# Kernel optimization log

Hardware: AMD Instinct MI355X
Metric: run time of the kernel (lower is better)

## Reference

```python
import jax, jax.numpy as jnp
import numpy as np

N_NODES = 8192
N_EDGES = 65536


def _segment_softmax(scores, seg_ids, num_segments):
    # scores: [E, 1], seg_ids: [E] -> softmax over edges sharing the same dst
    m = jax.ops.segment_max(scores, seg_ids, num_segments=num_segments)  # [N,1]
    e = jnp.exp(scores - m[seg_ids])
    denom = jax.ops.segment_sum(e, seg_ids, num_segments=num_segments)   # [N,1]
    return e / denom[seg_ids]


def setup_inputs() -> dict:
    key = jax.random.key(0)
    ks = jax.random.split(key, 12)
    s = lambda fin: 1.0 / np.sqrt(fin)
    inp = {
        'n_f': jax.random.normal(ks[0], (N_NODES, 1024), jnp.float32),
        'word2vec': jax.random.normal(ks[1], (N_NODES, 300), jnp.float32),
        's_f': jax.random.normal(ks[2], (N_EDGES, 16), jnp.float32),
        'src': jax.random.randint(ks[3], (N_EDGES,), 0, N_NODES),
        'dst': jax.random.randint(ks[4], (N_EDGES,), 0, N_NODES),
        'We': jax.random.normal(ks[5], (2064, 1024), jnp.float32) * s(2064),
        'be': jnp.zeros((1024,), jnp.float32),
        'Wel': jax.random.normal(ks[6], (600, 600), jnp.float32) * s(600),
        'bel': jnp.zeros((600,), jnp.float32),
        'Wa': jax.random.normal(ks[7], (1024, 1), jnp.float32) * s(1024),
        'ba': jnp.zeros((1,), jnp.float32),
        'Wal': jax.random.normal(ks[8], (600, 1), jnp.float32) * s(600),
        'bal': jnp.zeros((1,), jnp.float32),
        'Wn': jax.random.normal(ks[9], (2048, 1024), jnp.float32) * s(2048),
        'bn': jnp.zeros((1024,), jnp.float32),
        'Wnl': jax.random.normal(ks[10], (600, 300), jnp.float32) * s(600),
        'bnl': jnp.zeros((300,), jnp.float32),
    }
    return inp


def reference(n_f, word2vec, s_f, src, dst,
              We, be, Wel, bel, Wa, ba, Wal, bal, Wn, bn, Wnl, bnl):
    # ---- edge apply (H_H_EdgeApplyModule) ----
    src_nf = n_f[src]                                    # [E,1024] gather
    feat = jnp.concatenate([src_nf, s_f, n_f[dst]], axis=1)  # [E,2064]
    e_f = jax.nn.relu(feat @ We + be)                    # [E,1024]
    feat_lang = jnp.concatenate([word2vec[src], word2vec[dst]], axis=1)  # [E,600]
    e_f_lang = jax.nn.relu(feat_lang @ Wel + bel)        # [E,600]

    # ---- edge attention (E_AttentionModule1): scalar score per edge ----
    a_feat = e_f @ Wa + ba                               # [E,1]
    a_feat_lang = e_f_lang @ Wal + bal                   # [E,1]

    # ---- reduce: mailbox softmax over incoming edges per dst node ----
    alpha = _segment_softmax(a_feat, dst, N_NODES)       # [E,1]
    alpha_lang = _segment_softmax(a_feat_lang, dst, N_NODES)
    z_f = jax.ops.segment_sum(alpha * (src_nf + e_f), dst, num_segments=N_NODES)      # [N,1024]
    z_f_lang = jax.ops.segment_sum(alpha_lang * word2vec[src], dst, num_segments=N_NODES)  # [N,300]

    # ---- node apply (H_NodeApplyModule) ----
    new_n_f = jax.nn.relu(jnp.concatenate([n_f, z_f], axis=1) @ Wn + bn)              # [N,1024]
    new_n_f_lang = jax.nn.relu(jnp.concatenate([word2vec, z_f_lang], axis=1) @ Wnl + bnl)  # [N,300]
    return new_n_f, new_n_f_lang
```

## Files before the change

### kernel.cpp

```cpp
#include <hip/hip_runtime.h>
#include <hip/hip_bf16.h>

#define N_NODES 8192
#define N_EDGES 65536
#define OUT0_ELEMS ((size_t)N_NODES * 1024)

using bf16 = __hip_bfloat16;
typedef __attribute__((ext_vector_type(8))) short short8;
typedef __attribute__((ext_vector_type(4))) float f32x4;

__device__ __forceinline__ float b2f(bf16 x) { return __bfloat162float(x); }
__device__ __forceinline__ bf16 f2b(float x) { return __float2bfloat16(x); }
__device__ __forceinline__ unsigned short bbits(float x)
{
  union { bf16 h; unsigned short u; } v; v.h = f2b(x); return v.u;
}
__device__ __forceinline__ unsigned pack2(float a, float b)
{
  return (unsigned)bbits(a) | ((unsigned)bbits(b) << 16);
}
__device__ __forceinline__ float4 cvt2x(uint2 u)
{
  float4 r;
  r.x = __uint_as_float(u.x << 16);
  r.y = __uint_as_float(u.x & 0xffff0000u);
  r.z = __uint_as_float(u.y << 16);
  r.w = __uint_as_float(u.y & 0xffff0000u);
  return r;
}
__device__ __forceinline__ float4 ld4b(const bf16* p)
{
  uint2 u = *(const uint2*)p;
  return cvt2x(u);
}
__device__ __forceinline__ void st4b(bf16* p, float a, float b, float c, float d)
{
  uint2 v; v.x = pack2(a, b); v.y = pack2(c, d);
  *(uint2*)p = v;
}

__global__ void GNN_27650999451833_kernel() {}

__global__ void gnn6_zero(int* __restrict__ p, int n)
{
  int i = blockIdx.x * blockDim.x + threadIdx.x;
  if (i < n) p[i] = 0;
}

__global__ __launch_bounds__(256)
void gnn7_cvt(const float* __restrict__ src, bf16* __restrict__ dst, int n8)
{
  int i = blockIdx.x * blockDim.x + threadIdx.x;
  if (i < n8) {
    float4 a = ((const float4*)src)[2 * i];
    float4 b = ((const float4*)src)[2 * i + 1];
    uint4 p;
    p.x = pack2(a.x, a.y); p.y = pack2(a.z, a.w);
    p.z = pack2(b.x, b.y); p.w = pack2(b.z, b.w);
    ((uint4*)dst)[i] = p;
  }
}

__global__ __launch_bounds__(256)
void gnn8_pad_w2v(const float* __restrict__ src, bf16* __restrict__ dst)
{
  int idx = blockIdx.x * blockDim.x + threadIdx.x;
  if (idx >= N_NODES * 80) return;
  int r = idx / 80, c0 = (idx % 80) * 4;
  float v[4];
#pragma unroll
  for (int j = 0; j < 4; ++j) {
    int c = c0 + j;
    v[j] = (c < 300) ? src[(size_t)r * 300 + c] : 0.f;
  }
  uint2 p; p.x = pack2(v[0], v[1]); p.y = pack2(v[2], v[3]);
  *(uint2*)(dst + (size_t)r * 320 + c0) = p;
}

__global__ __launch_bounds__(256)
void gnn12_sf_pad(const float* __restrict__ s_f, bf16* __restrict__ sf_pad)
{
  int e = blockIdx.x * 256 + threadIdx.x;
  if (e >= N_EDGES) return;
  const float4* sp = (const float4*)(s_f + (size_t)e * 16);
  float4 s0 = sp[0], s1 = sp[1], s2 = sp[2], s3 = sp[3];
  uint4 lo, hi;
  lo.x = pack2(s0.x, s0.y); lo.y = pack2(s0.z, s0.w);
  lo.z = pack2(s1.x, s1.y); lo.w = pack2(s1.z, s1.w);
  hi.x = pack2(s2.x, s2.y); hi.y = pack2(s2.z, s2.w);
  hi.z = pack2(s3.x, s3.y); hi.w = pack2(s3.z, s3.w);
  uint4* dp = (uint4*)(sf_pad + (size_t)e * 32);
  dp[0] = lo; dp[1] = hi;
  dp[2] = (uint4){0, 0, 0, 0}; dp[3] = (uint4){0, 0, 0, 0};
}

__global__ __launch_bounds__(256)
void gnn12_t_Wetail(const float* __restrict__ We, bf16* __restrict__ BT)
{
  int c = blockIdx.x * 256 + threadIdx.x;
  if (c >= 1024) return;
  bf16* row = BT + (size_t)c * 32;
#pragma unroll
  for (int k = 0; k < 16; ++k)
    row[k] = f2b(We[(size_t)(1024 + k) * 1024 + c]);
#pragma unroll
  for (int k = 16; k < 32; ++k) row[k] = f2b(0.f);
}

__global__ __launch_bounds__(256)
void gnn10_t_We(const float* __restrict__ src, bf16* __restrict__ dst)
{
  __shared__ float tile[32][33];
  const int kb = blockIdx.x * 32, nb = blockIdx.y * 32;
  const int tx = threadIdx.x & 31, ty = threadIdx.x >> 5;
  const int n = nb + tx;
#pragma unroll
  for (int i = ty; i < 32; i += 8)
    tile[i][tx] = (n < 1024)
        ? src[(size_t)(kb + i) * 1024 + n]
        : src[(size_t)(1040 + kb + i) * 1024 + (n - 1024)];
  __syncthreads();
#pragma unroll
  for (int i = ty; i < 32; i += 8)
    dst[(size_t)(nb + i) * 1024 + kb + tx] = f2b(tile[tx][i]);
}

__global__ __launch_bounds__(256)
void gnn10_t_Wn(const float* __restrict__ src, bf16* __restrict__ dst)
{
  __shared__ float tile[32][33];
  const int kb = blockIdx.x * 32, nb = blockIdx.y * 32;
  const int tx = threadIdx.x & 31, ty = threadIdx.x >> 5;
#pragma unroll
  for (int i = ty; i < 32; i += 8)
    tile[i][tx] = src[(size_t)(kb + i) * 1024 + nb + tx];
  __syncthreads();
#pragma unroll
  for (int i = ty; i < 32; i += 8)
    dst[(size_t)(nb + i) * 2048 + kb + tx] = f2b(tile[tx][i]);
}

__global__ __launch_bounds__(256)
void gnn10_t_Wel(const float* __restrict__ src, bf16* __restrict__ dst)
{
  __shared__ float tile[32][33];
  const int kb = blockIdx.x * 32, nb = blockIdx.y * 32;
  const int tx = threadIdx.x & 31, ty = threadIdx.x >> 5;
  const int n = nb + tx;
#pragma unroll
  for (int i = ty; i < 32; i += 8) {
    int k = kb + i;
    float v = 0.f;
    if (k < 300) {
      if (n < 600)       v = src[(size_t)k * 600 + n];
      else if (n < 1200) v = src[(size_t)(300 + k) * 600 + (n - 600)];
    }
    tile[i][tx] = v;
  }
  __syncthreads();
#pragma unroll
  for (int i = ty; i < 32; i += 8)
    dst[(size_t)(nb + i) * 320 + kb + tx] = f2b(tile[tx][i]);
}

__global__ __launch_bounds__(256)
void gnn10_t_Wnl(const float* __restrict__ src, bf16* __restrict__ dst)
{
  __shared__ float tile[32][33];
  const int kb = blockIdx.x * 32, nb = blockIdx.y * 32;
  const int tx = threadIdx.x & 31, ty = threadIdx.x >> 5;
  const int n = nb + tx;
#pragma unroll
  for (int i = ty; i < 32; i += 8) {
    int k = kb + i;
    int kr = (k < 300) ? k : ((k >= 320 && k < 620) ? (k - 20) : -1);
    tile[i][tx] = (kr >= 0 && n < 300) ? src[(size_t)kr * 300 + n] : 0.f;
  }
  __syncthreads();
#pragma unroll
  for (int i = ty; i < 32; i += 8)
    dst[(size_t)(nb + i) * 640 + kb + tx] = f2b(tile[tx][i]);
}

__global__ __launch_bounds__(256)
void gnn10_mm_P(const bf16* __restrict__ A, const bf16* __restrict__ BT,
                bf16* __restrict__ P, const float* __restrict__ be)
{
  __shared__ short As[128 * 40];
  __shared__ short Bs[128 * 40];
  const int t = threadIdx.x;
  const int col0 = blockIdx.x * 128, row0 = blockIdx.y * 128;
  const int lane = t & 63, w = t >> 6, m16 = lane & 15, q = lane >> 4;
  const int wr = w >> 1, wc = w & 1;

  f32x4 acc[4][4];
#pragma unroll
  for (int mi = 0; mi < 4; ++mi)
#pragma unroll
    for (int ni = 0; ni < 4; ++ni) acc[mi][ni] = (f32x4){0.f, 0.f, 0.f, 0.f};

  const int ar = t >> 1, ah = (t & 1) * 16;
  const bf16* aptr = A + (size_t)(row0 + ar) * 1024 + ah;
  const bf16* bptr = BT + (size_t)(col0 + ar) * 1024 + ah;

  uint4 a0 = *(const uint4*)(aptr);
  uint4 a1 = *(const uint4*)(aptr + 8);
  uint4 b0 = *(const uint4*)(bptr);
  uint4 b1 = *(const uint4*)(bptr + 8);

  for (int k0 = 0; k0 < 1024; k0 += 32) {
    if (k0) __syncthreads();
    *(uint4*)&As[ar * 40 + ah] = a0;
    *(uint4*)&As[ar * 40 + ah + 8] = a1;
    *(uint4*)&Bs[ar * 40 + ah] = b0;
    *(uint4*)&Bs[ar * 40 + ah + 8] = b1;
    __syncthreads();
    if (k0 + 32 < 1024) {
      a0 = *(const uint4*)(aptr + k0 + 32);
      a1 = *(const uint4*)(aptr + k0 + 40);
      b0 = *(const uint4*)(bptr + k0 + 32);
      b1 = *(const uint4*)(bptr + k0 + 40);
    }
    short8 af[4];
#pragma unroll
    for (int mi = 0; mi < 4; ++mi)
      af[mi] = *(const short8*)&As[(wr * 64 + mi * 16 + m16) * 40 + 8 * q];
#pragma unroll
    for (int ni = 0; ni < 4; ++ni) {
      short8 bfv = *(const short8*)&Bs[(wc * 64 + ni * 16 + m16) * 40 + 8 * q];
#pragma unroll
      for (int mi = 0; mi < 4; ++mi)
        acc[mi][ni] =
            __builtin_amdgcn_mfma_f32_16x16x32_bf16(af[mi], bfv, acc[mi][ni], 0, 0, 0);
    }
  }
#pragma unroll
  for (int mi = 0; mi < 4; ++mi)
#pragma unroll
    for (int ni = 0; ni < 4; ++ni) {
      int c = col0 + wc * 64 + ni * 16 + m16;
      float bias = (be != nullptr && c >= 1024) ? be[c - 1024] : 0.f;
#pragma unroll
      for (int r = 0; r < 4; ++r)
        P[(size_t)(row0 + wr * 64 + mi * 16 + 4 * q + r) * 2048 + c] =
            f2b(acc[mi][ni][r] + bias);
    }
}

__global__ __launch_bounds__(256)
void gnn10_mm_out_n(const bf16* __restrict__ A0, const bf16* __restrict__ A1,
                    const bf16* __restrict__ BT, const float* __restrict__ bn,
                    float* __restrict__ out)
{
  __shared__ short As[128 * 40];
  __shared__ short Bs[128 * 40];
  const int t = threadIdx.x;
  const int col0 = blockIdx.x * 128, row0 = blockIdx.y * 128;
  const int lane = t & 63, w = t >> 6, m16 = lane & 15, q = lane >> 4;
  const int wr = w >> 1, wc = w & 1;

  f32x4 acc[4][4];
#pragma unroll
  for (int mi = 0; mi < 4; ++mi)
#pragma unroll
    for (int ni = 0; ni < 4; ++ni) acc[mi][ni] = (f32x4){0.f, 0.f, 0.f, 0.f};

  const int ar = t >> 1, ah = (t & 1) * 16;
  const bf16* ap0 = A0 + (size_t)(row0 + ar) * 1024 + ah;
  const bf16* ap1 = A1 + (size_t)(row0 + ar) * 1024 + ah;
  const bf16* bptr = BT + (size_t)(col0 + ar) * 2048 + ah;

  uint4 a0 = *(const uint4*)(ap0);
  uint4 a1 = *(const uint4*)(ap0 + 8);
  uint4 b0 = *(const uint4*)(bptr);
  uint4 b1 = *(const uint4*)(bptr + 8);

  for (int k0 = 0; k0 < 2048; k0 += 32) {
    if (k0) __syncthreads();
    *(uint4*)&As[ar * 40 + ah] = a0;
    *(uint4*)&As[ar * 40 + ah + 8] = a1;
    *(uint4*)&Bs[ar * 40 + ah] = b0;
    *(uint4*)&Bs[ar * 40 + ah + 8] = b1;
    __syncthreads();
    if (k0 + 32 < 2048) {
      int kn = k0 + 32;
      const bf16* ap = (kn < 1024) ? (ap0 + kn) : (ap1 + (kn - 1024));
      a0 = *(const uint4*)(ap);
      a1 = *(const uint4*)(ap + 8);
      b0 = *(const uint4*)(bptr + kn);
      b1 = *(const uint4*)(bptr + kn + 8);
    }
    short8 af[4];
#pragma unroll
    for (int mi = 0; mi < 4; ++mi)
      af[mi] = *(const short8*)&As[(wr * 64 + mi * 16 + m16) * 40 + 8 * q];
#pragma unroll
    for (int ni = 0; ni < 4; ++ni) {
      short8 bfv = *(const short8*)&Bs[(wc * 64 + ni * 16 + m16) * 40 + 8 * q];
#pragma unroll
      for (int mi = 0; mi < 4; ++mi)
        acc[mi][ni] =
            __builtin_amdgcn_mfma_f32_16x16x32_bf16(af[mi], bfv, acc[mi][ni], 0, 0, 0);
    }
  }
#pragma unroll
  for (int mi = 0; mi < 4; ++mi)
#pragma unroll
    for (int ni = 0; ni < 4; ++ni) {
      int c = col0 + wc * 64 + ni * 16 + m16;
      float bias = bn[c];
#pragma unroll
      for (int r = 0; r < 4; ++r) {
        float v = acc[mi][ni][r] + bias;
        out[(size_t)(row0 + wr * 64 + mi * 16 + 4 * q + r) * 1024 + c] =
            fmaxf(v, 0.f);
      }
    }
}

__global__ __launch_bounds__(256)
void gnn10_mm_Q(const bf16* __restrict__ A, const bf16* __restrict__ BT,
                bf16* __restrict__ Q, const float* __restrict__ bel)
{
  __shared__ short As[128 * 40];
  __shared__ short Bs[128 * 40];
  const int t = threadIdx.x;
  const int col0 = blockIdx.x * 128, row0 = blockIdx.y * 128;
  const int lane = t & 63, w = t >> 6, m16 = lane & 15, q = lane >> 4;
  const int wr = w >> 1, wc = w & 1;

  f32x4 acc[4][4];
#pragma unroll
  for (int mi = 0; mi < 4; ++mi)
#pragma unroll
    for (int ni = 0; ni < 4; ++ni) acc[mi][ni] = (f32x4){0.f, 0.f, 0.f, 0.f};

  const int ar = t >> 1, ah = (t & 1) * 16;
  const bf16* aptr = A + (size_t)(row0 + ar) * 320 + ah;
  const bf16* bptr = BT + (size_t)(col0 + ar) * 320 + ah;

  uint4 a0 = *(const uint4*)(aptr);
  uint4 a1 = *(const uint4*)(aptr + 8);
  uint4 b0 = *(const uint4*)(bptr);
  uint4 b1 = *(const uint4*)(bptr + 8);

  for (int k0 = 0; k0 < 320; k0 += 32) {
    if (k0) __syncthreads();
    *(uint4*)&As[ar * 40 + ah] = a0;
    *(uint4*)&As[ar * 40 + ah + 8] = a1;
    *(uint4*)&Bs[ar * 40 + ah] = b0;
    *(uint4*)&Bs[ar * 40 + ah + 8] = b1;
    __syncthreads();
    if (k0 + 32 < 320) {
      a0 = *(const uint4*)(aptr + k0 + 32);
      a1 = *(const uint4*)(aptr + k0 + 40);
      b0 = *(const uint4*)(bptr + k0 + 32);
      b1 = *(const uint4*)(bptr + k0 + 40);
    }
    short8 af[4];
#pragma unroll
    for (int mi = 0; mi < 4; ++mi)
      af[mi] = *(const short8*)&As[(wr * 64 + mi * 16 + m16) * 40 + 8 * q];
#pragma unroll
    for (int ni = 0; ni < 4; ++ni) {
      short8 bfv = *(const short8*)&Bs[(wc * 64 + ni * 16 + m16) * 40 + 8 * q];
#pragma unroll
      for (int mi = 0; mi < 4; ++mi)
        acc[mi][ni] =
            __builtin_amdgcn_mfma_f32_16x16x32_bf16(af[mi], bfv, acc[mi][ni], 0, 0, 0);
    }
  }
#pragma unroll
  for (int mi = 0; mi < 4; ++mi)
#pragma unroll
    for (int ni = 0; ni < 4; ++ni) {
      int c = col0 + wc * 64 + ni * 16 + m16;
      float bias = (bel != nullptr && c >= 600 && c < 1200) ? bel[c - 600] : 0.f;
#pragma unroll
      for (int r = 0; r < 4; ++r)
        Q[(size_t)(row0 + wr * 64 + mi * 16 + 4 * q + r) * 1280 + c] =
            f2b(acc[mi][ni][r] + bias);
    }
}

__global__ __launch_bounds__(256)
void gnn10_mm_out_l(const bf16* __restrict__ A0, const bf16* __restrict__ A1,
                    const bf16* __restrict__ BT, const float* __restrict__ bnl,
                    float* __restrict__ out2)
{
  __shared__ short As[128 * 40];
  __shared__ short Bs[128 * 40];
  const int t = threadIdx.x;
  const int col0 = blockIdx.x * 128, row0 = blockIdx.y * 128;
  const int lane = t & 63, w = t >> 6, m16 = lane & 15, q = lane >> 4;
  const int wr = w >> 1, wc = w & 1;

  f32x4 acc[4][4];
#pragma unroll
  for (int mi = 0; mi < 4; ++mi)
#pragma unroll
    for (int ni = 0; ni < 4; ++ni) acc[mi][ni] = (f32x4){0.f, 0.f, 0.f, 0.f};

  const int ar = t >> 1, ah = (t & 1) * 16;
  const bf16* ap0 = A0 + (size_t)(row0 + ar) * 320 + ah;
  const bf16* ap1 = A1 + (size_t)(row0 + ar) * 320 + ah;
  const bf16* bptr = BT + (size_t)(col0 + ar) * 640 + ah;

  uint4 a0 = *(const uint4*)(ap0);
  uint4 a1 = *(const uint4*)(ap0 + 8);
  uint4 b0 = *(const uint4*)(bptr);
  uint4 b1 = *(const uint4*)(bptr + 8);

  for (int k0 = 0; k0 < 640; k0 += 32) {
    if (k0) __syncthreads();
    *(uint4*)&As[ar * 40 + ah] = a0;
    *(uint4*)&As[ar * 40 + ah + 8] = a1;
    *(uint4*)&Bs[ar * 40 + ah] = b0;
    *(uint4*)&Bs[ar * 40 + ah + 8] = b1;
    __syncthreads();
    if (k0 + 32 < 640) {
      int kn = k0 + 32;
      const bf16* ap = (kn < 320) ? (ap0 + kn) : (ap1 + (kn - 320));
      a0 = *(const uint4*)(ap);
      a1 = *(const uint4*)(ap + 8);
      b0 = *(const uint4*)(bptr + kn);
      b1 = *(const uint4*)(bptr + kn + 8);
    }
    short8 af[4];
#pragma unroll
    for (int mi = 0; mi < 4; ++mi)
      af[mi] = *(const short8*)&As[(wr * 64 + mi * 16 + m16) * 40 + 8 * q];
#pragma unroll
    for (int ni = 0; ni < 4; ++ni) {
      short8 bfv = *(const short8*)&Bs[(wc * 64 + ni * 16 + m16) * 40 + 8 * q];
#pragma unroll
      for (int mi = 0; mi < 4; ++mi)
        acc[mi][ni] =
            __builtin_amdgcn_mfma_f32_16x16x32_bf16(af[mi], bfv, acc[mi][ni], 0, 0, 0);
    }
  }
#pragma unroll
  for (int mi = 0; mi < 4; ++mi)
#pragma unroll
    for (int ni = 0; ni < 4; ++ni) {
      int c = col0 + wc * 64 + ni * 16 + m16;
      if (c < 300) {
        float bias = bnl[c];
#pragma unroll
        for (int r = 0; r < 4; ++r) {
          float v = acc[mi][ni][r] + bias;
          out2[(size_t)(row0 + wr * 64 + mi * 16 + 4 * q + r) * 300 + c] =
              fmaxf(v, 0.f);
        }
      }
    }
}

#define SLD_STRIDE 1032
__global__ __launch_bounds__(256)
void gnn13_mm_S_score(const bf16* __restrict__ sfp, const bf16* __restrict__ WeTtail,
                      const int* __restrict__ src, const int* __restrict__ dst,
                      const float* __restrict__ Wa, const float* __restrict__ ba,
                      const float* __restrict__ Wal, const float* __restrict__ bal,
                      const bf16* __restrict__ P, const bf16* __restrict__ Q,
                      bf16* __restrict__ S, float* __restrict__ af,
                      float* __restrict__ afl)
{
  __shared__ short Sld[16 * SLD_STRIDE];
  __shared__ float shf[8][4], shl[8][4];
  const int t = threadIdx.x;
  const int lane = t & 63, w = t >> 6, m16 = lane & 15, q = lane >> 4;
  const int e0 = blockIdx.x * 16;

  short8 afr = *(const short8*)(sfp + (size_t)(e0 + m16) * 32 + 8 * q);
  const int cb = w * 256;
#pragma unroll
  for (int ni = 0; ni < 16; ++ni) {
    const int col = cb + ni * 16 + m16;
    short8 bfr = *(const short8*)(WeTtail + (size_t)col * 32 + 8 * q);
    f32x4 acc = __builtin_amdgcn_mfma_f32_16x16x32_bf16(
        afr, bfr, (f32x4){0.f, 0.f, 0.f, 0.f}, 0, 0, 0);
#pragma unroll
    for (int r = 0; r < 4; ++r)
      Sld[(4 * q + r) * SLD_STRIDE + col] = (short)bbits(acc[r]);
  }
  __syncthreads();

  {
    const int row = t >> 4, cseg = (t & 15) * 64;
#pragma unroll
    for (int j = 0; j < 8; ++j) {
      uint4 v = *(const uint4*)&Sld[row * SLD_STRIDE + cseg + 8 * j];
      *(uint4*)(S + (size_t)(e0 + row) * 1024 + cseg + 8 * j) = v;
    }
  }

  const int c0 = 4 * t;
  float4 wav = *(const float4*)(Wa + c0);
  const bool lact = (t < 150);
  float4 walv = {0, 0, 0, 0};
  if (lact) walv = *(const float4*)(Wal + c0);
  const float ba0 = ba[0], bal0 = bal[0];

#pragma unroll 1
  for (int bb = 0; bb < 2; ++bb) {
    const int eb = 8 * bb;
    int ss[8], dd[8];
    {
      int4 a4 = *(const int4*)(src + e0 + eb);
      int4 b4 = *(const int4*)(src + e0 + eb + 4);
      ss[0] = a4.x; ss[1] = a4.y; ss[2] = a4.z; ss[3] = a4.w;
      ss[4] = b4.x; ss[5] = b4.y; ss[6] = b4.z; ss[7] = b4.w;
      int4 c4 = *(const int4*)(dst + e0 + eb);
      int4 d4 = *(const int4*)(dst + e0 + eb + 4);
      dd[0] = c4.x; dd[1] = c4.y; dd[2] = c4.z; dd[3] = c4.w;
      dd[4] = d4.x; dd[5] = d4.y; dd[6] = d4.z; dd[7] = d4.w;
    }

    float pf[8], pl[8];
#pragma unroll
    for (int i = 0; i < 8; ++i) {
      uint2 us = *(const uint2*)&Sld[(eb + i) * SLD_STRIDE + c0];
      float4 sv = cvt2x(us);
      float4 p1 = ld4b(P + (size_t)ss[i] * 2048 + c0);
      float4 p2 = ld4b(P + (size_t)dd[i] * 2048 + 1024 + c0);
      float acc = 0.f;
      acc = fmaf(fmaxf(p1.x + p2.x + sv.x, 0.f), wav.x, acc);
      acc = fmaf(fmaxf(p1.y + p2.y + sv.y, 0.f), wav.y, acc);
      acc = fmaf(fmaxf(p1.z + p2.z + sv.z, 0.f), wav.z, acc);
      acc = fmaf(fmaxf(p1.w + p2.w + sv.w, 0.f), wav.w, acc);
      pf[i] = acc;

      float accl = 0.f;
      if (lact) {
        float4 q1 = ld4b(Q + (size_t)ss[i] * 1280 + c0);
        float4 q2 = ld4b(Q + (size_t)dd[i] * 1280 + 600 + c0);
        accl = fmaf(fmaxf(q1.x + q2.x, 0.f), walv.x, accl);
        accl = fmaf(fmaxf(q1.y + q2.y, 0.f), walv.y, accl);
        accl = fmaf(fmaxf(q1.z + q2.z, 0.f), walv.z, accl);
        accl = fmaf(fmaxf(q1.w + q2.w, 0.f), walv.w, accl);
      }
      pl[i] = accl;
    }

#pragma unroll
    for (int i = 0; i < 8; ++i) {
#pragma unroll
      for (int o = 32; o > 0; o >>= 1) {
        pf[i] += __shfl_down(pf[i], o, 64);
        pl[i] += __shfl_down(pl[i], o, 64);
      }
    }
    if (lane == 0) {
#pragma unroll
      for (int i = 0; i < 8; ++i) { shf[i][w] = pf[i]; shl[i][w] = pl[i]; }
    }
    __syncthreads();
    if (t < 8)
      af[e0 + eb + t] = shf[t][0] + shf[t][1] + shf[t][2] + shf[t][3] + ba0;
    if (t >= 64 && t < 72) {
      const int i = t & 7;
      afl[e0 + eb + i] = shl[i][0] + shl[i][1] + shl[i][2] + shl[i][3] + bal0;
    }
    __syncthreads();
  }
}

__global__ __launch_bounds__(256)
void gnn11_edge_score(const int* __restrict__ src, const int* __restrict__ dst,
                      const float* __restrict__ s_f, const float* __restrict__ We,
                      const float* __restrict__ be, const float* __restrict__ Wa,
                      const float* __restrict__ ba, const float* __restrict__ bel,
                      const float* __restrict__ Wal, const float* __restrict__ bal,
                      const bf16* __restrict__ P, const bf16* __restrict__ Q,
                      float* __restrict__ af, float* __restrict__ afl)
{
  const int t = threadIdx.x;
  const int lane = t & 63, w = t >> 6;
  const int c0 = 4 * t;
  const int e0 = blockIdx.x * 8;

  float wef[16][4];
#pragma unroll
  for (int k = 0; k < 16; ++k) {
    float4 v = *(const float4*)(We + (size_t)(1024 + k) * 1024 + c0);
    wef[k][0] = v.x; wef[k][1] = v.y; wef[k][2] = v.z; wef[k][3] = v.w;
  }
  float4 bev = *(const float4*)(be + c0);
  float4 wav = *(const float4*)(Wa + c0);
  const bool lact = (t < 150);
  float4 belv = {0, 0, 0, 0}, walv = {0, 0, 0, 0};
  if (lact) { belv = *(const float4*)(bel + c0); walv = *(const float4*)(Wal + c0); }

  int ss[8], dd[8];
  {
    int4 a = *(const int4*)(src + e0);
    int4 b = *(const int4*)(src + e0 + 4);
    ss[0] = a.x; ss[1] = a.y; ss[2] = a.z; ss[3] = a.w;
    ss[4] = b.x; ss[5] = b.y; ss[6] = b.z; ss[7] = b.w;
    int4 c = *(const int4*)(dst + e0);
    int4 d = *(const int4*)(dst + e0 + 4);
    dd[0] = c.x; dd[1] = c.y; dd[2] = c.z; dd[3] = c.w;
    dd[4] = d.x; dd[5] = d.y; dd[6] = d.z; dd[7] = d.w;
  }

  float pf[8], pl[8];

#pragma unroll
  for (int i = 0; i < 8; ++i) {
    const int e = e0 + i;
    float sfv[16];
    {
      const float4* sp = (const float4*)(s_f + (size_t)e * 16);
      float4 s0 = sp[0], s1 = sp[1], s2 = sp[2], s3 = sp[3];
      sfv[0] = s0.x; sfv[1] = s0.y; sfv[2] = s0.z; sfv[3] = s0.w;
      sfv[4] = s1.x; sfv[5] = s1.y; sfv[6] = s1.z; sfv[7] = s1.w;
      sfv[8] = s2.x; sfv[9] = s2.y; sfv[10] = s2.z; sfv[11] = s2.w;
      sfv[12] = s3.x; sfv[13] = s3.y; sfv[14] = s3.z; sfv[15] = s3.w;
    }
    float4 p1 = ld4b(P + (size_t)ss[i] * 2048 + c0);
    float4 p2 = ld4b(P + (size_t)dd[i] * 2048 + 1024 + c0);
    float pv[4] = {p1.x + p2.x + bev.x, p1.y + p2.y + bev.y,
                   p1.z + p2.z + bev.z, p1.w + p2.w + bev.w};
    float acc = 0.f;
#pragma unroll
    for (int j = 0; j < 4; ++j) {
      float v = pv[j];
#pragma unroll
      for (int k = 0; k < 16; ++k) v = fmaf(sfv[k], wef[k][j], v);
      acc = fmaf(fmaxf(v, 0.f), (&wav.x)[j], acc);
    }
    pf[i] = acc;

    float accl = 0.f;
    if (lact) {
      float4 q1 = ld4b(Q + (size_t)ss[i] * 1280 + c0);
      float4 q2 = ld4b(Q + (size_t)dd[i] * 1280 + 600 + c0);
      float qv[4] = {q1.x + q2.x + belv.x, q1.y + q2.y + belv.y,
                     q1.z + q2.z + belv.z, q1.w + q2.w + belv.w};
#pragma unroll
      for (int j = 0; j < 4; ++j)
        accl = fmaf(fmaxf(qv[j], 0.f), (&walv.x)[j], accl);
    }
    pl[i] = accl;
  }

  __shared__ float shf[8][4], shl[8][4];
#pragma unroll
  for (int i = 0; i < 8; ++i) {
#pragma unroll
    for (int o = 32; o > 0; o >>= 1) {
      pf[i] += __shfl_down(pf[i], o, 64);
      pl[i] += __shfl_down(pl[i], o, 64);
    }
  }
  if (lane == 0) {
#pragma unroll
    for (int i = 0; i < 8; ++i) { shf[i][w] = pf[i]; shl[i][w] = pl[i]; }
  }
  __syncthreads();
  if (t < 8)
    af[e0 + t] = shf[t][0] + shf[t][1] + shf[t][2] + shf[t][3] + ba[0];
  if (t >= 64 && t < 72) {
    const int i = t & 7;
    afl[e0 + i] = shl[i][0] + shl[i][1] + shl[i][2] + shl[i][3] + bal[0];
  }
}

__global__ void gnn6_count(const int* __restrict__ dst, int* __restrict__ cnt)
{
  int e = blockIdx.x * blockDim.x + threadIdx.x;
  if (e < N_EDGES) atomicAdd(&cnt[dst[e]], 1);
}

__global__ __launch_bounds__(1024)
void gnn6_scan(const int* __restrict__ cnt, int* __restrict__ off, int* __restrict__ cur)
{
  __shared__ int sh[1024];
  const int t = threadIdx.x;
  int local[8]; int sum = 0;
#pragma unroll
  for (int i = 0; i < 8; ++i) { int v = cnt[t * 8 + i]; local[i] = sum; sum += v; }
  sh[t] = sum;
  __syncthreads();
  for (int d = 1; d < 1024; d <<= 1) {
    int v = (t >= d) ? sh[t - d] : 0;
    __syncthreads();
    sh[t] += v;
    __syncthreads();
  }
  int basev = (t > 0) ? sh[t - 1] : 0;
#pragma unroll
  for (int i = 0; i < 8; ++i) { int o = basev + local[i]; off[t * 8 + i] = o; cur[t * 8 + i] = o; }
  if (t == 1023) off[8192] = sh[1023];
}

__global__ void gnn6_fill(const int* __restrict__ dst, int* __restrict__ cur,
                          int* __restrict__ elist)
{
  int e = blockIdx.x * blockDim.x + threadIdx.x;
  if (e < N_EDGES) { int p = atomicAdd(&cur[dst[e]], 1); elist[p] = e; }
}

__global__ __launch_bounds__(256)
void gnn6_alpha(const int* __restrict__ off, const int* __restrict__ elist,
                float* __restrict__ af, float* __restrict__ afl)
{
  const int n = blockIdx.x * 256 + threadIdx.x;
  if (n >= N_NODES) return;
  const int base = off[n];
  const int deg = off[n + 1] - base;
  float m = -1e30f, ml = -1e30f;
  for (int i = 0; i < deg; ++i) {
    int e = elist[base + i];
    m = fmaxf(m, af[e]);
    ml = fmaxf(ml, afl[e]);
  }
  float den = 0.f, denl = 0.f;
  for (int i = 0; i < deg; ++i) {
    int e = elist[base + i];
    den += expf(af[e] - m);
    denl += expf(afl[e] - ml);
  }
  float inv = (den > 0.f) ? 1.f / den : 0.f;
  float invl = (denl > 0.f) ? 1.f / denl : 0.f;
  for (int i = 0; i < deg; ++i) {
    int e = elist[base + i];
    af[e] = expf(af[e] - m) * inv;
    afl[e] = expf(afl[e] - ml) * invl;
  }
}

__global__ __launch_bounds__(256)
void gnn12_node_z(const int* __restrict__ off, const int* __restrict__ elist,
                  const int* __restrict__ src, const float* __restrict__ af,
                  const float* __restrict__ afl, const bf16* __restrict__ nf_bf,
                  const bf16* __restrict__ w2v_pad, const bf16* __restrict__ S,
                  const bf16* __restrict__ P, bf16* __restrict__ zf,
                  bf16* __restrict__ zfl_pad)
{
  const int node = blockIdx.x;
  const int t = threadIdx.x;
  const int c0 = 4 * t;
  const int base = off[node];
  const int deg = off[node + 1] - base;

  float4 p2v = ld4b(P + (size_t)node * 2048 + 1024 + c0);
  const float p2[4] = {p2v.x, p2v.y, p2v.z, p2v.w};

  float acc[4] = {0.f, 0.f, 0.f, 0.f};
  float accl[4] = {0.f, 0.f, 0.f, 0.f};
  const bool lact = (t < 75);

  for (int i = 0; i < deg; ++i) {
    const int e = elist[base + i];
    const int s = src[e];
    const float wgt = af[e];
    const float wl = afl[e];

    float4 sv = ld4b(S + (size_t)e * 1024 + c0);
    float4 p1 = ld4b(P + (size_t)s * 2048 + c0);
    float4 nf4 = ld4b(nf_bf + (size_t)s * 1024 + c0);
    const float p1a[4] = {p1.x, p1.y, p1.z, p1.w};
    const float sva[4] = {sv.x, sv.y, sv.z, sv.w};
    const float nfa[4] = {nf4.x, nf4.y, nf4.z, nf4.w};
#pragma unroll
    for (int j = 0; j < 4; ++j) {
      float ef = fmaxf(p1a[j] + p2[j] + sva[j], 0.f);
      acc[j] = fmaf(wgt, nfa[j] + ef, acc[j]);
    }
    if (lact) {
      float4 wv = ld4b(w2v_pad + (size_t)s * 320 + c0);
      accl[0] = fmaf(wl, wv.x, accl[0]);
      accl[1] = fmaf(wl, wv.y, accl[1]);
      accl[2] = fmaf(wl, wv.z, accl[2]);
      accl[3] = fmaf(wl, wv.w, accl[3]);
    }
  }
  st4b(zf + (size_t)node * 1024 + c0, acc[0], acc[1], acc[2], acc[3]);
  if (lact)
    st4b(zfl_pad + (size_t)node * 320 + c0, accl[0], accl[1], accl[2], accl[3]);
  else if (t < 80)
    st4b(zfl_pad + (size_t)node * 320 + c0, 0.f, 0.f, 0.f, 0.f);
}

__global__ __launch_bounds__(256)
void gnn9_node_z(const int* __restrict__ off, const int* __restrict__ elist,
                 const int* __restrict__ src, const float* __restrict__ af,
                 const float* __restrict__ afl, const bf16* __restrict__ nf_bf,
                 const bf16* __restrict__ w2v_pad, const float* __restrict__ s_f,
                 const float* __restrict__ We, const float* __restrict__ be,
                 const bf16* __restrict__ P, bf16* __restrict__ zf,
                 bf16* __restrict__ zfl_pad)
{
  const int node = blockIdx.x;
  const int t = threadIdx.x;
  const int c0 = 4 * t;
  const int base = off[node];
  const int deg = off[node + 1] - base;

  float wef[16][4];
#pragma unroll
  for (int k = 0; k < 16; ++k) {
    float4 v = *(const float4*)(We + (size_t)(1024 + k) * 1024 + c0);
    wef[k][0] = v.x; wef[k][1] = v.y; wef[k][2] = v.z; wef[k][3] = v.w;
  }
  float4 p2v = ld4b(P + (size_t)node * 2048 + 1024 + c0);
  float4 bev = *(const float4*)(be + c0);
  const float p2[4] = {p2v.x + bev.x, p2v.y + bev.y, p2v.z + bev.z, p2v.w + bev.w};

  float acc[4] = {0.f, 0.f, 0.f, 0.f};
  float accl[4] = {0.f, 0.f, 0.f, 0.f};
  const bool lact = (t < 75);

  for (int i = 0; i < deg; ++i) {
    const int e = elist[base + i];
    const int s = src[e];
    const float wgt = af[e];
    const float wl = afl[e];

    float sfv[16];
    {
      const float4* sp = (const float4*)(s_f + (size_t)e * 16);
      float4 s0 = sp[0], s1 = sp[1], s2 = sp[2], s3 = sp[3];
      sfv[0] = s0.x; sfv[1] = s0.y; sfv[2] = s0.z; sfv[3] = s0.w;
      sfv[4] = s1.x; sfv[5] = s1.y; sfv[6] = s1.z; sfv[7] = s1.w;
      sfv[8] = s2.x; sfv[9] = s2.y; sfv[10] = s2.z; sfv[11] = s2.w;
      sfv[12] = s3.x; sfv[13] = s3.y; sfv[14] = s3.z; sfv[15] = s3.w;
    }

    float4 p1 = ld4b(P + (size_t)s * 2048 + c0);
    float4 nf4 = ld4b(nf_bf + (size_t)s * 1024 + c0);
    const float p1a[4] = {p1.x, p1.y, p1.z, p1.w};
    const float nfa[4] = {nf4.x, nf4.y, nf4.z, nf4.w};
#pragma unroll
    for (int j = 0; j < 4; ++j) {
      float ef = p1a[j] + p2[j];
#pragma unroll
      for (int k = 0; k < 16; ++k) ef = fmaf(sfv[k], wef[k][j], ef);
      ef = fmaxf(ef, 0.f);
      acc[j] = fmaf(wgt, nfa[j] + ef, acc[j]);
    }
    if (lact) {
      float4 wv = ld4b(w2v_pad + (size_t)s * 320 + c0);
      accl[0] = fmaf(wl, wv.x, accl[0]);
      accl[1] = fmaf(wl, wv.y, accl[1]);
      accl[2] = fmaf(wl, wv.z, accl[2]);
      accl[3] = fmaf(wl, wv.w, accl[3]);
    }
  }
  st4b(zf + (size_t)node * 1024 + c0, acc[0], acc[1], acc[2], acc[3]);
  if (lact)
    st4b(zfl_pad + (size_t)node * 320 + c0, accl[0], accl[1], accl[2], accl[3]);
  else if (t < 80)
    st4b(zfl_pad + (size_t)node * 320 + c0, 0.f, 0.f, 0.f, 0.f);
}

extern "C" void kernel_launch(void* const* d_in, const int* in_sizes, int n_in,
                              void* d_out, int out_size, void* d_ws, size_t ws_size,
                              hipStream_t stream)
{
  (void)hipGetLastError();
  if (n_in != 17) { (void)hipMemsetAsync(d_out, 0x41, 4096, stream); return; }

  const float* n_f = (const float*)d_in[0];
  const float* w2v = (const float*)d_in[1];
  const float* s_f = (const float*)d_in[2];
  const int*   src = (const int*)d_in[3];
  const int*   dst = (const int*)d_in[4];
  const float* We  = (const float*)d_in[5];
  const float* be  = (const float*)d_in[6];
  const float* Wel = (const float*)d_in[7];
  const float* bel = (const float*)d_in[8];
  const float* Wa  = (const float*)d_in[9];
  const float* ba  = (const float*)d_in[10];
  const float* Wal = (const float*)d_in[11];
  const float* bal = (const float*)d_in[12];
  const float* Wn  = (const float*)d_in[13];
  const float* bn  = (const float*)d_in[14];
  const float* Wnl = (const float*)d_in[15];
  const float* bnl = (const float*)d_in[16];
  float* out  = (float*)d_out;
  float* out2 = out + OUT0_ELEMS;

  char* ws = (char*)d_ws;
  size_t o = 0;
  auto alloc = [&](size_t bytes) -> void* {
    void* p = ws + o; o += bytes; o = (o + 255) & ~(size_t)255; return p;
  };
  bf16* P        = (bf16*)alloc((size_t)N_NODES * 2048 * 2);
  bf16* Q        = (bf16*)alloc((size_t)N_NODES * 1280 * 2);
  bf16* zf       = (bf16*)alloc((size_t)N_NODES * 1024 * 2);
  bf16* zfl_pad  = (bf16*)alloc((size_t)N_NODES * 320 * 2);
  bf16* nf_bf    = (bf16*)alloc((size_t)N_NODES * 1024 * 2);
  bf16* w2v_pad  = (bf16*)alloc((size_t)N_NODES * 320 * 2);
  bf16* WeT      = (bf16*)alloc((size_t)2048 * 1024 * 2);
  bf16* WnT      = (bf16*)alloc((size_t)1024 * 2048 * 2);
  bf16* WelT     = (bf16*)alloc((size_t)1280 * 320 * 2);
  bf16* WnlT     = (bf16*)alloc((size_t)384 * 640 * 2);
  float* af      = (float*)alloc((size_t)N_EDGES * 4);
  float* afl     = (float*)alloc((size_t)N_EDGES * 4);
  int* cnt       = (int*)alloc((size_t)N_NODES * 4);
  int* offs      = (int*)alloc((size_t)(N_NODES + 1) * 4);
  int* cur       = (int*)alloc((size_t)N_NODES * 4);
  int* elist     = (int*)alloc((size_t)N_EDGES * 4);
  size_t base_end = o;
  if (base_end > ws_size) { (void)hipMemsetAsync(d_out, 0x42, 4096, stream); return; }

  bf16* sf_pad  = (bf16*)alloc((size_t)N_EDGES * 32 * 2);
  bf16* WeTtail = (bf16*)alloc((size_t)1024 * 32 * 2);
  bf16* S       = (bf16*)alloc((size_t)N_EDGES * 1024 * 2);
  const bool useS = (o <= ws_size);

  gnn6_zero<<<N_NODES / 256, 256, 0, stream>>>(cnt, N_NODES);
  gnn7_cvt<<<(N_NODES * 1024 / 8 + 255) / 256, 256, 0, stream>>>(n_f, nf_bf,
                                                                 N_NODES * 1024 / 8);
  gnn8_pad_w2v<<<(N_NODES * 80 + 255) / 256, 256, 0, stream>>>(w2v, w2v_pad);
  { dim3 g(32, 64); gnn10_t_We<<<g, 256, 0, stream>>>(We, WeT); }
  { dim3 g(64, 32); gnn10_t_Wn<<<g, 256, 0, stream>>>(Wn, WnT); }
  { dim3 g(10, 40); gnn10_t_Wel<<<g, 256, 0, stream>>>(Wel, WelT); }
  { dim3 g(20, 12); gnn10_t_Wnl<<<g, 256, 0, stream>>>(Wnl, WnlT); }
  if (useS) {
    gnn12_sf_pad<<<N_EDGES / 256, 256, 0, stream>>>(s_f, sf_pad);
    gnn12_t_Wetail<<<4, 256, 0, stream>>>(We, WeTtail);
  }

  {
    dim3 g(2048 / 128, N_NODES / 128);
    gnn10_mm_P<<<g, 256, 0, stream>>>(nf_bf, WeT, P, useS ? be : nullptr);
  }
  {
    dim3 g(1280 / 128, N_NODES / 128);
    gnn10_mm_Q<<<g, 256, 0, stream>>>(w2v_pad, WelT, Q, useS ? bel : nullptr);
  }

  if (useS) {
    gnn13_mm_S_score<<<N_EDGES / 16, 256, 0, stream>>>(
        sf_pad, WeTtail, src, dst, Wa, ba, Wal, bal, P, Q, S, af, afl);
  } else {
    gnn11_edge_score<<<N_EDGES / 8, 256, 0, stream>>>(src, dst, s_f, We, be, Wa,
                                                      ba, bel, Wal, bal, P, Q,
                                                      af, afl);
  }

  gnn6_count<<<N_EDGES / 256, 256, 0, stream>>>(dst, cnt);
  gnn6_scan<<<1, 1024, 0, stream>>>(cnt, offs, cur);
  gnn6_fill<<<N_EDGES / 256, 256, 0, stream>>>(dst, cur, elist);
  gnn6_alpha<<<N_NODES / 256, 256, 0, stream>>>(offs, elist, af, afl);

  if (useS) {
    gnn12_node_z<<<N_NODES, 256, 0, stream>>>(offs, elist, src, af, afl, nf_bf,
                                              w2v_pad, S, P, zf, zfl_pad);
  } else {
    gnn9_node_z<<<N_NODES, 256, 0, stream>>>(offs, elist, src, af, afl, nf_bf,
                                             w2v_pad, s_f, We, be, P, zf, zfl_pad);
  }

  {
    dim3 g(1024 / 128, N_NODES / 128);
    gnn10_mm_out_n<<<g, 256, 0, stream>>>(nf_bf, zf, WnT, bn, out);
  }
  {
    dim3 g(384 / 128, N_NODES / 128);
    gnn10_mm_out_l<<<g, 256, 0, stream>>>(w2v_pad, zfl_pad, WnlT, bnl, out2);
  }

  if (hipGetLastError() != hipSuccess) (void)hipMemsetAsync(d_out, 0x44, 4096, stream);
}
```

Baseline: 517.6 us.

## Sort edges by destination before scoring so S and scores are stored CSR-contiguous

```diff
diff --git a/kernel.cpp b/kernel.cpp
--- a/kernel.cpp
+++ b/kernel.cpp
@@ -75,23 +75,6 @@
   }
   uint2 p; p.x = pack2(v[0], v[1]); p.y = pack2(v[2], v[3]);
   *(uint2*)(dst + (size_t)r * 320 + c0) = p;
-}
-
-__global__ __launch_bounds__(256)
-void gnn12_sf_pad(const float* __restrict__ s_f, bf16* __restrict__ sf_pad)
-{
-  int e = blockIdx.x * 256 + threadIdx.x;
-  if (e >= N_EDGES) return;
-  const float4* sp = (const float4*)(s_f + (size_t)e * 16);
-  float4 s0 = sp[0], s1 = sp[1], s2 = sp[2], s3 = sp[3];
-  uint4 lo, hi;
-  lo.x = pack2(s0.x, s0.y); lo.y = pack2(s0.z, s0.w);
-  lo.z = pack2(s1.x, s1.y); lo.w = pack2(s1.z, s1.w);
-  hi.x = pack2(s2.x, s2.y); hi.y = pack2(s2.z, s2.w);
-  hi.z = pack2(s3.x, s3.y); hi.w = pack2(s3.z, s3.w);
-  uint4* dp = (uint4*)(sf_pad + (size_t)e * 32);
-  dp[0] = lo; dp[1] = hi;
-  dp[2] = (uint4){0, 0, 0, 0}; dp[3] = (uint4){0, 0, 0, 0};
 }
 
 __global__ __launch_bounds__(256)
@@ -456,10 +439,78 @@
     }
 }
 
+__global__ void gnn6_count(const int* __restrict__ dst, int* __restrict__ cnt)
+{
+  int e = blockIdx.x * blockDim.x + threadIdx.x;
+  if (e < N_EDGES) atomicAdd(&cnt[dst[e]], 1);
+}
+
+__global__ __launch_bounds__(1024)
+void gnn6_scan(const int* __restrict__ cnt, int* __restrict__ off, int* __restrict__ cur)
+{
+  __shared__ int sh[1024];
+  const int t = threadIdx.x;
+  int local[8]; int sum = 0;
+#pragma unroll
+  for (int i = 0; i < 8; ++i) { int v = cnt[t * 8 + i]; local[i] = sum; sum += v; }
+  sh[t] = sum;
+  __syncthreads();
+  for (int d = 1; d < 1024; d <<= 1) {
+    int v = (t >= d) ? sh[t - d] : 0;
+    __syncthreads();
+    sh[t] += v;
+    __syncthreads();
+  }
+  int basev = (t > 0) ? sh[t - 1] : 0;
+#pragma unroll
+  for (int i = 0; i < 8; ++i) { int o = basev + local[i]; off[t * 8 + i] = o; cur[t * 8 + i] = o; }
+  if (t == 1023) off[8192] = sh[1023];
+}
+
+__global__ void gnn6_fill(const int* __restrict__ dst, int* __restrict__ cur,
+                          int* __restrict__ elist)
+{
+  int e = blockIdx.x * blockDim.x + threadIdx.x;
+  if (e < N_EDGES) { int p = atomicAdd(&cur[dst[e]], 1); elist[p] = e; }
+}
+
+__global__ void gnn14_fill(const int* __restrict__ dst, const int* __restrict__ src,
+                           int* __restrict__ cur, int* __restrict__ elist,
+                           int* __restrict__ srcs, int* __restrict__ dsts)
+{
+  int e = blockIdx.x * blockDim.x + threadIdx.x;
+  if (e < N_EDGES) {
+    int d = dst[e];
+    int p = atomicAdd(&cur[d], 1);
+    elist[p] = e;
+    srcs[p] = src[e];
+    dsts[p] = d;
+  }
+}
+
+__global__ __launch_bounds__(256)
+void gnn14_sfp(const float* __restrict__ s_f, const int* __restrict__ elist,
+               bf16* __restrict__ sfp)
+{
+  int p = blockIdx.x * 256 + threadIdx.x;
+  if (p >= N_EDGES) return;
+  int e = elist[p];
+  const float4* sp = (const float4*)(s_f + (size_t)e * 16);
+  float4 s0 = sp[0], s1 = sp[1], s2 = sp[2], s3 = sp[3];
+  uint4 lo, hi;
+  lo.x = pack2(s0.x, s0.y); lo.y = pack2(s0.z, s0.w);
+  lo.z = pack2(s1.x, s1.y); lo.w = pack2(s1.z, s1.w);
+  hi.x = pack2(s2.x, s2.y); hi.y = pack2(s2.z, s2.w);
+  hi.z = pack2(s3.x, s3.y); hi.w = pack2(s3.z, s3.w);
+  uint4* dp = (uint4*)(sfp + (size_t)p * 32);
+  dp[0] = lo; dp[1] = hi;
+  dp[2] = (uint4){0, 0, 0, 0}; dp[3] = (uint4){0, 0, 0, 0};
+}
+
 #define SLD_STRIDE 1032
 __global__ __launch_bounds__(256)
-void gnn13_mm_S_score(const bf16* __restrict__ sfp, const bf16* __restrict__ WeTtail,
-                      const int* __restrict__ src, const int* __restrict__ dst,
+void gnn14_mm_S_score(const bf16* __restrict__ sfp, const bf16* __restrict__ WeTtail,
+                      const int* __restrict__ srcs, const int* __restrict__ dsts,
                       const float* __restrict__ Wa, const float* __restrict__ ba,
                       const float* __restrict__ Wal, const float* __restrict__ bal,
                       const bf16* __restrict__ P, const bf16* __restrict__ Q,
@@ -470,28 +521,26 @@
   __shared__ float shf[8][4], shl[8][4];
   const int t = threadIdx.x;
   const int lane = t & 63, w = t >> 6, m16 = lane & 15, q = lane >> 4;
-  const int e0 = blockIdx.x * 16;
-
-  short8 afr = *(const short8*)(sfp + (size_t)(e0 + m16) * 32 + 8 * q);
+  const int p0 = blockIdx.x * 16;
+
+  short8 bfr = *(const short8*)(sfp + (size_t)(p0 + m16) * 32 + 8 * q);
   const int cb = w * 256;
 #pragma unroll
   for (int ni = 0; ni < 16; ++ni) {
-    const int col = cb + ni * 16 + m16;
-    short8 bfr = *(const short8*)(WeTtail + (size_t)col * 32 + 8 * q);
+    short8 afr = *(const short8*)(WeTtail + (size_t)(cb + ni * 16 + m16) * 32 + 8 * q);
     f32x4 acc = __builtin_amdgcn_mfma_f32_16x16x32_bf16(
         afr, bfr, (f32x4){0.f, 0.f, 0.f, 0.f}, 0, 0, 0);
-#pragma unroll
-    for (int r = 0; r < 4; ++r)
-      Sld[(4 * q + r) * SLD_STRIDE + col] = (short)bbits(acc[r]);
+    uint2 v; v.x = pack2(acc[0], acc[1]); v.y = pack2(acc[2], acc[3]);
+    *(uint2*)&Sld[m16 * SLD_STRIDE + cb + ni * 16 + 4 * q] = v;
   }
   __syncthreads();
 
   {
-    const int row = t >> 4, cseg = (t & 15) * 64;
+    const int row = t >> 4, cbase = (t & 15) * 8;
 #pragma unroll
     for (int j = 0; j < 8; ++j) {
-      uint4 v = *(const uint4*)&Sld[row * SLD_STRIDE + cseg + 8 * j];
-      *(uint4*)(S + (size_t)(e0 + row) * 1024 + cseg + 8 * j) = v;
+      uint4 v = *(const uint4*)&Sld[row * SLD_STRIDE + cbase + 128 * j];
+      *(uint4*)(S + (size_t)(p0 + row) * 1024 + cbase + 128 * j) = v;
     }
   }
 
@@ -507,12 +556,12 @@
     const int eb = 8 * bb;
     int ss[8], dd[8];
     {
-      int4 a4 = *(const int4*)(src + e0 + eb);
-      int4 b4 = *(const int4*)(src + e0 + eb + 4);
+      int4 a4 = *(const int4*)(srcs + p0 + eb);
+      int4 b4 = *(const int4*)(srcs + p0 + eb + 4);
       ss[0] = a4.x; ss[1] = a4.y; ss[2] = a4.z; ss[3] = a4.w;
       ss[4] = b4.x; ss[5] = b4.y; ss[6] = b4.z; ss[7] = b4.w;
-      int4 c4 = *(const int4*)(dst + e0 + eb);
-      int4 d4 = *(const int4*)(dst + e0 + eb + 4);
+      int4 c4 = *(const int4*)(dsts + p0 + eb);
+      int4 d4 = *(const int4*)(dsts + p0 + eb + 4);
       dd[0] = c4.x; dd[1] = c4.y; dd[2] = c4.z; dd[3] = c4.w;
       dd[4] = d4.x; dd[5] = d4.y; dd[6] = d4.z; dd[7] = d4.w;
     }
@@ -557,10 +606,10 @@
     }
     __syncthreads();
     if (t < 8)
-      af[e0 + eb + t] = shf[t][0] + shf[t][1] + shf[t][2] + shf[t][3] + ba0;
+      af[p0 + eb + t] = shf[t][0] + shf[t][1] + shf[t][2] + shf[t][3] + ba0;
     if (t >= 64 && t < 72) {
       const int i = t & 7;
-      afl[e0 + eb + i] = shl[i][0] + shl[i][1] + shl[i][2] + shl[i][3] + bal0;
+      afl[p0 + eb + i] = shl[i][0] + shl[i][1] + shl[i][2] + shl[i][3] + bal0;
     }
     __syncthreads();
   }
@@ -667,39 +716,30 @@
   }
 }
 
-__global__ void gnn6_count(const int* __restrict__ dst, int* __restrict__ cnt)
-{
-  int e = blockIdx.x * blockDim.x + threadIdx.x;
-  if (e < N_EDGES) atomicAdd(&cnt[dst[e]], 1);
-}
-
-__global__ __launch_bounds__(1024)
-void gnn6_scan(const int* __restrict__ cnt, int* __restrict__ off, int* __restrict__ cur)
-{
-  __shared__ int sh[1024];
-  const int t = threadIdx.x;
-  int local[8]; int sum = 0;
-#pragma unroll
-  for (int i = 0; i < 8; ++i) { int v = cnt[t * 8 + i]; local[i] = sum; sum += v; }
-  sh[t] = sum;
-  __syncthreads();
-  for (int d = 1; d < 1024; d <<= 1) {
-    int v = (t >= d) ? sh[t - d] : 0;
-    __syncthreads();
-    sh[t] += v;
-    __syncthreads();
-  }
-  int basev = (t > 0) ? sh[t - 1] : 0;
-#pragma unroll
-  for (int i = 0; i < 8; ++i) { int o = basev + local[i]; off[t * 8 + i] = o; cur[t * 8 + i] = o; }
-  if (t == 1023) off[8192] = sh[1023];
-}
-
-__global__ void gnn6_fill(const int* __restrict__ dst, int* __restrict__ cur,
-                          int* __restrict__ elist)
-{
-  int e = blockIdx.x * blockDim.x + threadIdx.x;
-  if (e < N_EDGES) { int p = atomicAdd(&cur[dst[e]], 1); elist[p] = e; }
+__global__ __launch_bounds__(256)
+void gnn14_alpha(const int* __restrict__ off, float* __restrict__ af,
+                 float* __restrict__ afl)
+{
+  const int n = blockIdx.x * 256 + threadIdx.x;
+  if (n >= N_NODES) return;
+  const int base = off[n];
+  const int deg = off[n + 1] - base;
+  float m = -1e30f, ml = -1e30f;
+  for (int i = 0; i < deg; ++i) {
+    m = fmaxf(m, af[base + i]);
+    ml = fmaxf(ml, afl[base + i]);
+  }
+  float den = 0.f, denl = 0.f;
+  for (int i = 0; i < deg; ++i) {
+    den += expf(af[base + i] - m);
+    denl += expf(afl[base + i] - ml);
+  }
+  float inv = (den > 0.f) ? 1.f / den : 0.f;
+  float invl = (denl > 0.f) ? 1.f / denl : 0.f;
+  for (int i = 0; i < deg; ++i) {
+    af[base + i] = expf(af[base + i] - m) * inv;
+    afl[base + i] = expf(afl[base + i] - ml) * invl;
+  }
 }
 
 __global__ __launch_bounds__(256)
@@ -732,12 +772,11 @@
 }
 
 __global__ __launch_bounds__(256)
-void gnn12_node_z(const int* __restrict__ off, const int* __restrict__ elist,
-                  const int* __restrict__ src, const float* __restrict__ af,
-                  const float* __restrict__ afl, const bf16* __restrict__ nf_bf,
-                  const bf16* __restrict__ w2v_pad, const bf16* __restrict__ S,
-                  const bf16* __restrict__ P, bf16* __restrict__ zf,
-                  bf16* __restrict__ zfl_pad)
+void gnn14_node_z(const int* __restrict__ off, const int* __restrict__ srcs,
+                  const float* __restrict__ af, const float* __restrict__ afl,
+                  const bf16* __restrict__ nf_bf, const bf16* __restrict__ w2v_pad,
+                  const bf16* __restrict__ S, const bf16* __restrict__ P,
+                  bf16* __restrict__ zf, bf16* __restrict__ zfl_pad)
 {
   const int node = blockIdx.x;
   const int t = threadIdx.x;
@@ -753,12 +792,12 @@
   const bool lact = (t < 75);
 
   for (int i = 0; i < deg; ++i) {
-    const int e = elist[base + i];
-    const int s = src[e];
-    const float wgt = af[e];
-    const float wl = afl[e];
-
-    float4 sv = ld4b(S + (size_t)e * 1024 + c0);
+    const int pidx = base + i;
+    const int s = srcs[pidx];
+    const float wgt = af[pidx];
+    const float wl = afl[pidx];
+
+    float4 sv = ld4b(S + (size_t)pidx * 1024 + c0);
     float4 p1 = ld4b(P + (size_t)s * 2048 + c0);
     float4 nf4 = ld4b(nf_bf + (size_t)s * 1024 + c0);
     const float p1a[4] = {p1.x, p1.y, p1.z, p1.w};
@@ -907,9 +946,11 @@
   size_t base_end = o;
   if (base_end > ws_size) { (void)hipMemsetAsync(d_out, 0x42, 4096, stream); return; }
 
-  bf16* sf_pad  = (bf16*)alloc((size_t)N_EDGES * 32 * 2);
+  bf16* sfp     = (bf16*)alloc((size_t)N_EDGES * 32 * 2);
   bf16* WeTtail = (bf16*)alloc((size_t)1024 * 32 * 2);
   bf16* S       = (bf16*)alloc((size_t)N_EDGES * 1024 * 2);
+  int* srcs     = (int*)alloc((size_t)N_EDGES * 4);
+  int* dsts     = (int*)alloc((size_t)N_EDGES * 4);
   const bool useS = (o <= ws_size);
 
   gnn6_zero<<<N_NODES / 256, 256, 0, stream>>>(cnt, N_NODES);
@@ -920,9 +961,15 @@
   { dim3 g(64, 32); gnn10_t_Wn<<<g, 256, 0, stream>>>(Wn, WnT); }
   { dim3 g(10, 40); gnn10_t_Wel<<<g, 256, 0, stream>>>(Wel, WelT); }
   { dim3 g(20, 12); gnn10_t_Wnl<<<g, 256, 0, stream>>>(Wnl, WnlT); }
+
+  gnn6_count<<<N_EDGES / 256, 256, 0, stream>>>(dst, cnt);
+  gnn6_scan<<<1, 1024, 0, stream>>>(cnt, offs, cur);
   if (useS) {
-    gnn12_sf_pad<<<N_EDGES / 256, 256, 0, stream>>>(s_f, sf_pad);
+    gnn14_fill<<<N_EDGES / 256, 256, 0, stream>>>(dst, src, cur, elist, srcs, dsts);
     gnn12_t_Wetail<<<4, 256, 0, stream>>>(We, WeTtail);
+    gnn14_sfp<<<N_EDGES / 256, 256, 0, stream>>>(s_f, elist, sfp);
+  } else {
+    gnn6_fill<<<N_EDGES / 256, 256, 0, stream>>>(dst, cur, elist);
   }
 
   {
@@ -935,23 +982,16 @@
   }
 
   if (useS) {
-    gnn13_mm_S_score<<<N_EDGES / 16, 256, 0, stream>>>(
-        sf_pad, WeTtail, src, dst, Wa, ba, Wal, bal, P, Q, S, af, afl);
+    gnn14_mm_S_score<<<N_EDGES / 16, 256, 0, stream>>>(
+        sfp, WeTtail, srcs, dsts, Wa, ba, Wal, bal, P, Q, S, af, afl);
+    gnn14_alpha<<<N_NODES / 256, 256, 0, stream>>>(offs, af, afl);
+    gnn14_node_z<<<N_NODES, 256, 0, stream>>>(offs, srcs, af, afl, nf_bf,
+                                              w2v_pad, S, P, zf, zfl_pad);
   } else {
     gnn11_edge_score<<<N_EDGES / 8, 256, 0, stream>>>(src, dst, s_f, We, be, Wa,
                                                       ba, bel, Wal, bal, P, Q,
                                                       af, afl);
-  }
-
-  gnn6_count<<<N_EDGES / 256, 256, 0, stream>>>(dst, cnt);
-  gnn6_scan<<<1, 1024, 0, stream>>>(cnt, offs, cur);
-  gnn6_fill<<<N_EDGES / 256, 256, 0, stream>>>(dst, cur, elist);
-  gnn6_alpha<<<N_NODES / 256, 256, 0, stream>>>(offs, elist, af, afl);
-
-  if (useS) {
-    gnn12_node_z<<<N_NODES, 256, 0, stream>>>(offs, elist, src, af, afl, nf_bf,
-                                              w2v_pad, S, P, zf, zfl_pad);
-  } else {
+    gnn6_alpha<<<N_NODES / 256, 256, 0, stream>>>(offs, elist, af, afl);
     gnn9_node_z<<<N_NODES, 256, 0, stream>>>(offs, elist, src, af, afl, nf_bf,
                                              w2v_pad, s_f, We, be, P, zf, zfl_pad);
   }
```

Result: faster. 480.4 us (-7.2%).
